# Performance work log

Measured on AMD Instinct MI355X. Metric: run time of the kernel, lower is better.

Reference implementation:

```python
import jax, jax.numpy as jnp
import numpy as np

STAGE_NUM = 3
BN_EPS = 1e-5


def _l2norm(x, axis):
    return x / (1e-6 + jnp.linalg.norm(x, axis=axis, keepdims=True))


def setup_inputs() -> dict:
    key = jax.random.key(0)
    b, c, k = 16, 256, 64
    sizes = [(80, 80), (40, 40), (20, 20), (10, 10)]
    ks = jax.random.split(key, 12)
    inp = {}
    for i, (h, w) in enumerate(sizes):
        inp[f"x{i}"] = jax.random.normal(ks[i], (b, c, h, w), dtype=jnp.float32)
    # 1x1 conv weights, kaiming-style init as in the module (n = out_channels)
    inp["w1"] = jax.random.normal(ks[8], (c, c), dtype=jnp.float32) * np.sqrt(2.0 / c)
    inp["b1"] = jnp.zeros((c,), dtype=jnp.float32)
    inp["w2"] = jax.random.normal(ks[9], (c, c), dtype=jnp.float32) * np.sqrt(2.0 / c)
    inp["bn_gamma"] = jnp.ones((c,), dtype=jnp.float32)
    inp["bn_beta"] = jnp.zeros((c,), dtype=jnp.float32)
    inp["bn_mean"] = jnp.zeros((c,), dtype=jnp.float32)
    inp["bn_var"] = jnp.ones((c,), dtype=jnp.float32)
    mu = jax.random.normal(ks[10], (1, c, k), dtype=jnp.float32) * np.sqrt(2.0 / k)
    inp["mu"] = _l2norm(mu, axis=1)
    return inp


def reference(x0, x1, x2, x3, w1, b1, w2, bn_gamma, bn_beta, bn_mean, bn_var, mu):
    xs = [x0, x1, x2, x3]
    b, c = x0.shape[0], x0.shape[1]
    idn = xs
    # conv1: 1x1 conv with bias == channel matmul
    xs = [jnp.einsum('oc,bchw->bohw', w1, x) + b1[None, :, None, None] for x in xs]
    sizes = [x.shape for x in xs]
    x_total = jnp.concatenate([x.reshape(b, c, -1) for x in xs], axis=-1)  # [b,c,N]
    k = mu.shape[-1]
    mu_b = jnp.broadcast_to(mu, (b, c, k))
    # EM iterations run under torch.no_grad() in the original -> stop_gradient
    xt = jax.lax.stop_gradient(x_total)
    z = None
    for _ in range(STAGE_NUM):
        z = jax.nn.softmax(jnp.einsum('bcn,bck->bnk', xt, mu_b), axis=2)  # [b,N,k]
        z_ = z / (1e-6 + z.sum(axis=1, keepdims=True))
        mu_b = _l2norm(jnp.einsum('bcn,bnk->bck', xt, z_), axis=1)
    # reconstruction: mu @ z^T, relu
    x_rec = jax.nn.relu(jnp.einsum('bck,bnk->bcn', mu_b, z))  # [b,c,N]
    outs = []
    cur = 0
    inv_std = (bn_gamma / jnp.sqrt(bn_var + BN_EPS))[None, :, None, None]
    shift = (bn_beta - bn_mean * bn_gamma / jnp.sqrt(bn_var + BN_EPS))[None, :, None, None]
    for i, s in enumerate(sizes):
        n = s[2] * s[3]
        term = x_rec[:, :, cur:cur + n].reshape(s)
        cur += n
        y = jnp.einsum('oc,bchw->bohw', w2, term)  # conv2 (no bias)
        y = y * inv_std + shift                    # eval-mode BatchNorm2d
        outs.append(jax.nn.relu(y + idn[i]))
    return (*outs, mu_b)
```

## Files before the change

kernel.cpp:

```cpp
#include <hip/hip_runtime.h>
#include <math.h>

#define NTOT 8500

__device__ __forceinline__ size_t in_index(int gn, int bc, int* which) {
  if (gn < 6400) { *which = 0; return (size_t)bc * 6400 + gn; }
  if (gn < 8000) { *which = 1; return (size_t)bc * 1600 + (gn - 6400); }
  if (gn < 8400) { *which = 2; return (size_t)bc * 400  + (gn - 8000); }
  *which = 3;     return (size_t)bc * 100  + (gn - 8400);
}

template <int WHICH>
__global__ __launch_bounds__(256)
void conv_kernel(const float* __restrict__ W, const float* __restrict__ bias,
                 const float* __restrict__ x0, const float* __restrict__ x1,
                 const float* __restrict__ x2, const float* __restrict__ x3,
                 const float* __restrict__ xrec,
                 const float* __restrict__ bn_g, const float* __restrict__ bn_b,
                 const float* __restrict__ bn_m, const float* __restrict__ bn_v,
                 float* __restrict__ out)
{
  __shared__ float As[32][68];
  __shared__ float Bs[32][132];
  const int t  = threadIdx.x;
  const int n0 = blockIdx.x * 128;
  const int m0 = blockIdx.y * 64;
  const int b  = blockIdx.z;
  const int tm = t & 15, tn = t >> 4;

  float acc[4][8];
#pragma unroll
  for (int i = 0; i < 4; ++i)
#pragma unroll
    for (int j = 0; j < 8; ++j) acc[i][j] = 0.f;

  for (int k0 = 0; k0 < 256; k0 += 32) {
#pragma unroll
    for (int it = 0; it < 2; ++it) {
      const int o_l = (t >> 3) + 32 * it;
      const int kk4 = (t & 7) * 4;
      float4 v = *(const float4*)(W + (size_t)(m0 + o_l) * 256 + k0 + kk4);
      As[kk4 + 0][o_l] = v.x; As[kk4 + 1][o_l] = v.y;
      As[kk4 + 2][o_l] = v.z; As[kk4 + 3][o_l] = v.w;
    }
#pragma unroll
    for (int it = 0; it < 4; ++it) {
      const int kk  = (t >> 5) + 8 * it;
      const int nn4 = (t & 31) * 4;
      const int gn  = n0 + nn4;
      float4 v = make_float4(0.f, 0.f, 0.f, 0.f);
      if (gn < NTOT) {
        if (WHICH == 0) {
          int w_; size_t idx = in_index(gn, b * 256 + k0 + kk, &w_);
          const float* src = (w_ == 0) ? x0 : (w_ == 1) ? x1 : (w_ == 2) ? x2 : x3;
          v = *(const float4*)(src + idx);
        } else {
          v = *(const float4*)(xrec + (size_t)(b * 256 + k0 + kk) * NTOT + gn);
        }
      }
      *(float4*)&Bs[kk][nn4] = v;
    }
    __syncthreads();
#pragma unroll
    for (int kk = 0; kk < 32; ++kk) {
      float4 a = *(const float4*)&As[kk][tm * 4];
      float4 p = *(const float4*)&Bs[kk][tn * 8];
      float4 q = *(const float4*)&Bs[kk][tn * 8 + 4];
      float av[4] = {a.x, a.y, a.z, a.w};
      float bv[8] = {p.x, p.y, p.z, p.w, q.x, q.y, q.z, q.w};
#pragma unroll
      for (int i = 0; i < 4; ++i)
#pragma unroll
        for (int j = 0; j < 8; ++j)
          acc[i][j] = fmaf(av[i], bv[j], acc[i][j]);
    }
    __syncthreads();
  }

#pragma unroll
  for (int i = 0; i < 4; ++i) {
    const int o = m0 + tm * 4 + i;
    float addb = 0.f, isf = 0.f, shf = 0.f;
    if (WHICH == 0) {
      addb = bias[o];
    } else {
      float g = bn_g[o];
      isf = g / sqrtf(bn_v[o] + 1e-5f);
      shf = bn_b[o] - bn_m[o] * isf;
    }
#pragma unroll
    for (int jj = 0; jj < 8; jj += 4) {
      const int gn = n0 + tn * 8 + jj;
      if (gn >= NTOT) continue;
      float4 r = make_float4(acc[i][jj + 0], acc[i][jj + 1],
                             acc[i][jj + 2], acc[i][jj + 3]);
      if (WHICH == 0) {
        r.x += addb; r.y += addb; r.z += addb; r.w += addb;
        *(float4*)(out + (size_t)(b * 256 + o) * NTOT + gn) = r;
      } else {
        int w_; size_t idx = in_index(gn, b * 256 + o, &w_);
        const float* src = (w_ == 0) ? x0 : (w_ == 1) ? x1 : (w_ == 2) ? x2 : x3;
        float4 rv = *(const float4*)(src + idx);
        size_t ob = (w_ == 0) ? 0ull : (w_ == 1) ? 26214400ull
                  : (w_ == 2) ? 32768000ull : 34406400ull;
        r.x = fmaxf(fmaf(r.x, isf, shf) + rv.x, 0.f);
        r.y = fmaxf(fmaf(r.y, isf, shf) + rv.y, 0.f);
        r.z = fmaxf(fmaf(r.z, isf, shf) + rv.z, 0.f);
        r.w = fmaxf(fmaf(r.w, isf, shf) + rv.w, 0.f);
        *(float4*)(out + ob + idx) = r;
      }
    }
  }
}

__global__ __launch_bounds__(256)
void z_kernel(const float* __restrict__ xt, const float* __restrict__ mu,
              int mu_per_batch, float* __restrict__ zbuf)
{
  __shared__ float xs[32][136];
  __shared__ float mus[32][68];
  const int t  = threadIdx.x;
  const int n0 = blockIdx.x * 128;
  const int b  = blockIdx.y;
  const float* mub = mu + (mu_per_batch ? (size_t)b * 256 * 64 : 0);
  const int tk = t & 15, tn = t >> 4;

  float acc[8][4];
#pragma unroll
  for (int r = 0; r < 8; ++r)
#pragma unroll
    for (int j = 0; j < 4; ++j) acc[r][j] = 0.f;

  for (int c0 = 0; c0 < 256; c0 += 32) {
#pragma unroll
    for (int it = 0; it < 4; ++it) {
      const int cc  = (t >> 5) + 8 * it;
      const int nn4 = (t & 31) * 4;
      const int gn  = n0 + nn4;
      float4 v = (gn < NTOT)
          ? *(const float4*)(xt + (size_t)(b * 256 + c0 + cc) * NTOT + gn)
          : make_float4(0.f, 0.f, 0.f, 0.f);
      *(float4*)&xs[cc][nn4] = v;
    }
#pragma unroll
    for (int it = 0; it < 2; ++it) {
      const int cc  = (t >> 4) + 16 * it;
      const int kk4 = (t & 15) * 4;
      float4 v = *(const float4*)(mub + (size_t)(c0 + cc) * 64 + kk4);
      *(float4*)&mus[cc][kk4] = v;
    }
    __syncthreads();
#pragma unroll
    for (int cc = 0; cc < 32; ++cc) {
      float4 m4 = *(const float4*)&mus[cc][tk * 4];
      float4 xa = *(const float4*)&xs[cc][tn * 8];
      float4 xb = *(const float4*)&xs[cc][tn * 8 + 4];
      float xv[8] = {xa.x, xa.y, xa.z, xa.w, xb.x, xb.y, xb.z, xb.w};
      float mv[4] = {m4.x, m4.y, m4.z, m4.w};
#pragma unroll
      for (int r = 0; r < 8; ++r)
#pragma unroll
        for (int j = 0; j < 4; ++j)
          acc[r][j] = fmaf(xv[r], mv[j], acc[r][j]);
    }
    __syncthreads();
  }

#pragma unroll
  for (int r = 0; r < 8; ++r) {
    float mx = fmaxf(fmaxf(acc[r][0], acc[r][1]), fmaxf(acc[r][2], acc[r][3]));
#pragma unroll
    for (int off = 8; off >= 1; off >>= 1) mx = fmaxf(mx, __shfl_xor(mx, off));
    float e0 = __expf(acc[r][0] - mx), e1 = __expf(acc[r][1] - mx);
    float e2 = __expf(acc[r][2] - mx), e3 = __expf(acc[r][3] - mx);
    float s = e0 + e1 + e2 + e3;
#pragma unroll
    for (int off = 8; off >= 1; off >>= 1) s += __shfl_xor(s, off);
    const float inv = 1.0f / s;
    const int gn = n0 + tn * 8 + r;
    if (gn < NTOT) {
      float4 w = make_float4(e0 * inv, e1 * inv, e2 * inv, e3 * inv);
      *(float4*)(zbuf + ((size_t)b * NTOT + gn) * 64 + tk * 4) = w;
    }
  }
}

__global__ __launch_bounds__(256)
void mu_part_kernel(const float* __restrict__ xt, const float* __restrict__ z,
                    float* __restrict__ part)
{
  __shared__ float As[32][132];
  __shared__ float Bs[32][68];
  const int t  = threadIdx.x;
  const int ch = blockIdx.x;
  const int c0 = blockIdx.y * 128;
  const int b  = blockIdx.z;
  const int nb = ch * 512;
  const int tk = t & 15, tc = t >> 4;

  float acc[8][4];
#pragma unroll
  for (int i = 0; i < 8; ++i)
#pragma unroll
    for (int j = 0; j < 4; ++j) acc[i][j] = 0.f;

  for (int kb = 0; kb < 512; kb += 32) {
#pragma unroll
    for (int it = 0; it < 4; ++it) {
      const int c_l = (t >> 3) + 32 * it;
      const int nn4 = (t & 7) * 4;
      const int gn  = nb + kb + nn4;
      float4 v = (gn < NTOT)
          ? *(const float4*)(xt + (size_t)(b * 256 + c0 + c_l) * NTOT + gn)
          : make_float4(0.f, 0.f, 0.f, 0.f);
      As[nn4 + 0][c_l] = v.x; As[nn4 + 1][c_l] = v.y;
      As[nn4 + 2][c_l] = v.z; As[nn4 + 3][c_l] = v.w;
    }
#pragma unroll
    for (int it = 0; it < 2; ++it) {
      const int nn  = (t >> 4) + 16 * it;
      const int kk4 = (t & 15) * 4;
      const int gn  = nb + kb + nn;
      float4 v = (gn < NTOT)
          ? *(const float4*)(z + ((size_t)b * NTOT + gn) * 64 + kk4)
          : make_float4(0.f, 0.f, 0.f, 0.f);
      *(float4*)&Bs[nn][kk4] = v;
    }
    __syncthreads();
#pragma unroll
    for (int nn = 0; nn < 32; ++nn) {
      float4 a0 = *(const float4*)&As[nn][tc * 8];
      float4 a1 = *(const float4*)&As[nn][tc * 8 + 4];
      float4 bz = *(const float4*)&Bs[nn][tk * 4];
      float av[8] = {a0.x, a0.y, a0.z, a0.w, a1.x, a1.y, a1.z, a1.w};
      float bv[4] = {bz.x, bz.y, bz.z, bz.w};
#pragma unroll
      for (int i = 0; i < 8; ++i)
#pragma unroll
        for (int j = 0; j < 4; ++j)
          acc[i][j] = fmaf(av[i], bv[j], acc[i][j]);
    }
    __syncthreads();
  }

#pragma unroll
  for (int j = 0; j < 4; ++j) {
    const int k = tk * 4 + j;
    float4 v0 = make_float4(acc[0][j], acc[1][j], acc[2][j], acc[3][j]);
    float4 v1 = make_float4(acc[4][j], acc[5][j], acc[6][j], acc[7][j]);
    size_t base = (((size_t)b * 17 + ch) * 64 + k) * 256 + c0 + tc * 8;
    *(float4*)(part + base)     = v0;
    *(float4*)(part + base + 4) = v1;
  }
}

__global__ __launch_bounds__(256)
void mu_reduce_kernel(const float* __restrict__ part, float* __restrict__ mu_ws,
                      float* __restrict__ mu_out)
{
  const int k = blockIdx.x;
  const int b = blockIdx.y;
  const int c = threadIdx.x;
  float s = 0.f;
  for (int ch = 0; ch < 17; ++ch)
    s += part[(((size_t)b * 17 + ch) * 64 + k) * 256 + c];
  __shared__ float red[256];
  red[c] = s * s;
  __syncthreads();
  for (int off = 128; off > 0; off >>= 1) {
    if (c < off) red[c] += red[c + off];
    __syncthreads();
  }
  const float f   = 1.0f / (1e-6f + sqrtf(red[0]));
  const float val = s * f;
  mu_ws[((size_t)b * 256 + c) * 64 + k] = val;
  if (mu_out) mu_out[((size_t)b * 256 + c) * 64 + k] = val;
}

__global__ __launch_bounds__(256)
void rec_kernel(const float* __restrict__ mu, const float* __restrict__ z,
                float* __restrict__ xrec)
{
  __shared__ float As[16][68];
  __shared__ float Bs[16][132];
  const int t  = threadIdx.x;
  const int n0 = blockIdx.x * 128;
  const int c0 = blockIdx.y * 64;
  const int b  = blockIdx.z;
  const int tm = t & 15, tn = t >> 4;

  float acc[4][8];
#pragma unroll
  for (int i = 0; i < 4; ++i)
#pragma unroll
    for (int j = 0; j < 8; ++j) acc[i][j] = 0.f;

  for (int k0 = 0; k0 < 64; k0 += 16) {
    {
      const int c_l = t >> 2;
      const int kk4 = (t & 3) * 4;
      float4 v = *(const float4*)(mu + ((size_t)(b * 256 + c0 + c_l)) * 64 + k0 + kk4);
      As[kk4 + 0][c_l] = v.x; As[kk4 + 1][c_l] = v.y;
      As[kk4 + 2][c_l] = v.z; As[kk4 + 3][c_l] = v.w;
    }
#pragma unroll
    for (int it = 0; it < 2; ++it) {
      const int nn  = (t >> 2) + 64 * it;
      const int kk4 = (t & 3) * 4;
      const int gn  = n0 + nn;
      float4 v = (gn < NTOT)
          ? *(const float4*)(z + ((size_t)b * NTOT + gn) * 64 + k0 + kk4)
          : make_float4(0.f, 0.f, 0.f, 0.f);
      Bs[kk4 + 0][nn] = v.x; Bs[kk4 + 1][nn] = v.y;
      Bs[kk4 + 2][nn] = v.z; Bs[kk4 + 3][nn] = v.w;
    }
    __syncthreads();
#pragma unroll
    for (int kk = 0; kk < 16; ++kk) {
      float4 a = *(const float4*)&As[kk][tm * 4];
      float4 p = *(const float4*)&Bs[kk][tn * 8];
      float4 q = *(const float4*)&Bs[kk][tn * 8 + 4];
      float av[4] = {a.x, a.y, a.z, a.w};
      float bv[8] = {p.x, p.y, p.z, p.w, q.x, q.y, q.z, q.w};
#pragma unroll
      for (int i = 0; i < 4; ++i)
#pragma unroll
        for (int j = 0; j < 8; ++j)
          acc[i][j] = fmaf(av[i], bv[j], acc[i][j]);
    }
    __syncthreads();
  }

#pragma unroll
  for (int i = 0; i < 4; ++i) {
    const int cc = c0 + tm * 4 + i;
#pragma unroll
    for (int jj = 0; jj < 8; jj += 4) {
      const int gn = n0 + tn * 8 + jj;
      if (gn >= NTOT) continue;
      float4 r = make_float4(fmaxf(acc[i][jj + 0], 0.f), fmaxf(acc[i][jj + 1], 0.f),
                             fmaxf(acc[i][jj + 2], 0.f), fmaxf(acc[i][jj + 3], 0.f));
      *(float4*)(xrec + (size_t)(b * 256 + cc) * NTOT + gn) = r;
    }
  }
}

extern "C" void kernel_launch(void* const* d_in, const int* in_sizes, int n_in,
                              void* d_out, int out_size, void* d_ws, size_t ws_size,
                              hipStream_t stream)
{
  const float* x0   = (const float*)d_in[0];
  const float* x1   = (const float*)d_in[1];
  const float* x2   = (const float*)d_in[2];
  const float* x3   = (const float*)d_in[3];
  const float* w1   = (const float*)d_in[4];
  const float* b1   = (const float*)d_in[5];
  const float* w2   = (const float*)d_in[6];
  const float* bn_g = (const float*)d_in[7];
  const float* bn_b = (const float*)d_in[8];
  const float* bn_m = (const float*)d_in[9];
  const float* bn_v = (const float*)d_in[10];
  const float* mu0  = (const float*)d_in[11];
  float* out = (float*)d_out;

  float* xt   = (float*)d_ws;
  float* z    = xt   + 34816000ull;
  float* part = z    + 8704000ull;
  float* muws = part + 4456448ull;

  dim3 gconv(67, 4, 16);
  conv_kernel<0><<<gconv, 256, 0, stream>>>(w1, b1, x0, x1, x2, x3,
                                            nullptr, nullptr, nullptr, nullptr,
                                            nullptr, xt);
  for (int s = 0; s < 3; ++s) {
    z_kernel<<<dim3(67, 16), 256, 0, stream>>>(xt, s == 0 ? mu0 : muws,
                                               s == 0 ? 0 : 1, z);
    mu_part_kernel<<<dim3(17, 2, 16), 256, 0, stream>>>(xt, z, part);
    mu_reduce_kernel<<<dim3(64, 16), 256, 0, stream>>>(
        part, muws, (s == 2) ? (out + 34816000ull) : nullptr);
  }
  rec_kernel<<<dim3(67, 4, 16), 256, 0, stream>>>(muws, z, xt);
  conv_kernel<1><<<gconv, 256, 0, stream>>>(w2, nullptr, x0, x1, x2, x3,
                                            xt, bn_g, bn_b, bn_m, bn_v, out);
}
```

Baseline: 1.232 ms.

## Eliminate conv1 by folding W1 and bias into EM projections

Removes the conv1 GEMM and its 139 MB xt intermediate. The EM iterations now work on the raw inputs. Scores use W1^T·mu plus a bias term, and mu updates apply W1 (plus b1 times the z column sums) to x·z. Small per-iteration kernels compute the transformed mu (t, s), and the column sums of z are accumulated inside mu_part. This trades a large GEMM and a full write/read of xt for extra small matvecs and gathers from the four input tensors, with slight changes in floating-point rounding.

Result: slower. 1.308 ms (+6.2%).

```diff
diff --git a/kernel.cpp b/kernel.cpp
--- a/kernel.cpp
+++ b/kernel.cpp
@@ -10,15 +10,14 @@
   *which = 3;     return (size_t)bc * 100  + (gn - 8400);
 }
 
-template <int WHICH>
-__global__ __launch_bounds__(256)
-void conv_kernel(const float* __restrict__ W, const float* __restrict__ bias,
-                 const float* __restrict__ x0, const float* __restrict__ x1,
-                 const float* __restrict__ x2, const float* __restrict__ x3,
-                 const float* __restrict__ xrec,
-                 const float* __restrict__ bn_g, const float* __restrict__ bn_b,
-                 const float* __restrict__ bn_m, const float* __restrict__ bn_v,
-                 float* __restrict__ out)
+__global__ __launch_bounds__(256)
+void conv2_kernel(const float* __restrict__ W,
+                  const float* __restrict__ x0, const float* __restrict__ x1,
+                  const float* __restrict__ x2, const float* __restrict__ x3,
+                  const float* __restrict__ xrec,
+                  const float* __restrict__ bn_g, const float* __restrict__ bn_b,
+                  const float* __restrict__ bn_m, const float* __restrict__ bn_v,
+                  float* __restrict__ out)
 {
   __shared__ float As[32][68];
   __shared__ float Bs[32][132];
@@ -49,15 +48,8 @@
       const int nn4 = (t & 31) * 4;
       const int gn  = n0 + nn4;
       float4 v = make_float4(0.f, 0.f, 0.f, 0.f);
-      if (gn < NTOT) {
-        if (WHICH == 0) {
-          int w_; size_t idx = in_index(gn, b * 256 + k0 + kk, &w_);
-          const float* src = (w_ == 0) ? x0 : (w_ == 1) ? x1 : (w_ == 2) ? x2 : x3;
-          v = *(const float4*)(src + idx);
-        } else {
-          v = *(const float4*)(xrec + (size_t)(b * 256 + k0 + kk) * NTOT + gn);
-        }
-      }
+      if (gn < NTOT)
+        v = *(const float4*)(xrec + (size_t)(b * 256 + k0 + kk) * NTOT + gn);
       *(float4*)&Bs[kk][nn4] = v;
     }
     __syncthreads();
@@ -80,50 +72,83 @@
 #pragma unroll
   for (int i = 0; i < 4; ++i) {
     const int o = m0 + tm * 4 + i;
-    float addb = 0.f, isf = 0.f, shf = 0.f;
-    if (WHICH == 0) {
-      addb = bias[o];
-    } else {
-      float g = bn_g[o];
-      isf = g / sqrtf(bn_v[o] + 1e-5f);
-      shf = bn_b[o] - bn_m[o] * isf;
-    }
+    float g   = bn_g[o];
+    float isf = g / sqrtf(bn_v[o] + 1e-5f);
+    float shf = bn_b[o] - bn_m[o] * isf;
 #pragma unroll
     for (int jj = 0; jj < 8; jj += 4) {
       const int gn = n0 + tn * 8 + jj;
       if (gn >= NTOT) continue;
       float4 r = make_float4(acc[i][jj + 0], acc[i][jj + 1],
                              acc[i][jj + 2], acc[i][jj + 3]);
-      if (WHICH == 0) {
-        r.x += addb; r.y += addb; r.z += addb; r.w += addb;
-        *(float4*)(out + (size_t)(b * 256 + o) * NTOT + gn) = r;
-      } else {
-        int w_; size_t idx = in_index(gn, b * 256 + o, &w_);
-        const float* src = (w_ == 0) ? x0 : (w_ == 1) ? x1 : (w_ == 2) ? x2 : x3;
-        float4 rv = *(const float4*)(src + idx);
-        size_t ob = (w_ == 0) ? 0ull : (w_ == 1) ? 26214400ull
-                  : (w_ == 2) ? 32768000ull : 34406400ull;
-        r.x = fmaxf(fmaf(r.x, isf, shf) + rv.x, 0.f);
-        r.y = fmaxf(fmaf(r.y, isf, shf) + rv.y, 0.f);
-        r.z = fmaxf(fmaf(r.z, isf, shf) + rv.z, 0.f);
-        r.w = fmaxf(fmaf(r.w, isf, shf) + rv.w, 0.f);
-        *(float4*)(out + ob + idx) = r;
-      }
-    }
-  }
-}
-
-__global__ __launch_bounds__(256)
-void z_kernel(const float* __restrict__ xt, const float* __restrict__ mu,
-              int mu_per_batch, float* __restrict__ zbuf)
+      int w_; size_t idx = in_index(gn, b * 256 + o, &w_);
+      const float* src = (w_ == 0) ? x0 : (w_ == 1) ? x1 : (w_ == 2) ? x2 : x3;
+      float4 rv = *(const float4*)(src + idx);
+      size_t ob = (w_ == 0) ? 0ull : (w_ == 1) ? 26214400ull
+                : (w_ == 2) ? 32768000ull : 34406400ull;
+      r.x = fmaxf(fmaf(r.x, isf, shf) + rv.x, 0.f);
+      r.y = fmaxf(fmaf(r.y, isf, shf) + rv.y, 0.f);
+      r.z = fmaxf(fmaf(r.z, isf, shf) + rv.z, 0.f);
+      r.w = fmaxf(fmaf(r.w, isf, shf) + rv.w, 0.f);
+      *(float4*)(out + ob + idx) = r;
+    }
+  }
+}
+
+__global__ __launch_bounds__(256)
+void transpose_kernel(const float* __restrict__ w1, float* __restrict__ w1t)
+{
+  __shared__ float tile[32][33];
+  const int bx = blockIdx.x, by = blockIdx.y;
+  const int tx = threadIdx.x & 31, ty = threadIdx.x >> 5;
+#pragma unroll
+  for (int j = 0; j < 32; j += 8)
+    tile[ty + j][tx] = w1[(size_t)(by * 32 + ty + j) * 256 + bx * 32 + tx];
+  __syncthreads();
+#pragma unroll
+  for (int j = 0; j < 32; j += 8)
+    w1t[(size_t)(bx * 32 + ty + j) * 256 + by * 32 + tx] = tile[tx][ty + j];
+}
+
+__global__ __launch_bounds__(256)
+void t0_kernel(const float* __restrict__ w1, const float* __restrict__ b1,
+               const float* __restrict__ mu0, float* __restrict__ t0,
+               float* __restrict__ s0)
+{
+  const int k = blockIdx.x, c = threadIdx.x;
+  __shared__ float M[256];
+  __shared__ float red[256];
+  M[c] = mu0[(size_t)c * 64 + k];
+  __syncthreads();
+  float acc = 0.f;
+#pragma unroll 8
+  for (int cp = 0; cp < 256; ++cp)
+    acc = fmaf(w1[(size_t)cp * 256 + c], M[cp], acc);
+  t0[(size_t)c * 64 + k] = acc;
+  red[c] = b1[c] * M[c];
+  __syncthreads();
+  for (int off = 128; off > 0; off >>= 1) {
+    if (c < off) red[c] += red[c + off];
+    __syncthreads();
+  }
+  if (c == 0) s0[k] = red[0];
+}
+
+__global__ __launch_bounds__(256)
+void z_kernel(const float* __restrict__ x0, const float* __restrict__ x1,
+              const float* __restrict__ x2, const float* __restrict__ x3,
+              const float* __restrict__ t, const float* __restrict__ s,
+              int per_batch, float* __restrict__ zbuf)
 {
   __shared__ float xs[32][136];
   __shared__ float mus[32][68];
-  const int t  = threadIdx.x;
+  const int tid = threadIdx.x;
   const int n0 = blockIdx.x * 128;
   const int b  = blockIdx.y;
-  const float* mub = mu + (mu_per_batch ? (size_t)b * 256 * 64 : 0);
-  const int tk = t & 15, tn = t >> 4;
+  const float* tb = t + (per_batch ? (size_t)b * 256 * 64 : 0);
+  const float* sb = s + (per_batch ? (size_t)b * 64 : 0);
+  const int tk = tid & 15, tn = tid >> 4;
+  const float4 sv = *(const float4*)(sb + tk * 4);
 
   float acc[8][4];
 #pragma unroll
@@ -134,19 +159,22 @@
   for (int c0 = 0; c0 < 256; c0 += 32) {
 #pragma unroll
     for (int it = 0; it < 4; ++it) {
-      const int cc  = (t >> 5) + 8 * it;
-      const int nn4 = (t & 31) * 4;
+      const int cc  = (tid >> 5) + 8 * it;
+      const int nn4 = (tid & 31) * 4;
       const int gn  = n0 + nn4;
-      float4 v = (gn < NTOT)
-          ? *(const float4*)(xt + (size_t)(b * 256 + c0 + cc) * NTOT + gn)
-          : make_float4(0.f, 0.f, 0.f, 0.f);
+      float4 v = make_float4(0.f, 0.f, 0.f, 0.f);
+      if (gn < NTOT) {
+        int w_; size_t idx = in_index(gn, b * 256 + c0 + cc, &w_);
+        const float* src = (w_ == 0) ? x0 : (w_ == 1) ? x1 : (w_ == 2) ? x2 : x3;
+        v = *(const float4*)(src + idx);
+      }
       *(float4*)&xs[cc][nn4] = v;
     }
 #pragma unroll
     for (int it = 0; it < 2; ++it) {
-      const int cc  = (t >> 4) + 16 * it;
-      const int kk4 = (t & 15) * 4;
-      float4 v = *(const float4*)(mub + (size_t)(c0 + cc) * 64 + kk4);
+      const int cc  = (tid >> 4) + 16 * it;
+      const int kk4 = (tid & 15) * 4;
+      float4 v = *(const float4*)(tb + (size_t)(c0 + cc) * 64 + kk4);
       *(float4*)&mus[cc][kk4] = v;
     }
     __syncthreads();
@@ -168,15 +196,16 @@
 
 #pragma unroll
   for (int r = 0; r < 8; ++r) {
+    acc[r][0] += sv.x; acc[r][1] += sv.y; acc[r][2] += sv.z; acc[r][3] += sv.w;
     float mx = fmaxf(fmaxf(acc[r][0], acc[r][1]), fmaxf(acc[r][2], acc[r][3]));
 #pragma unroll
     for (int off = 8; off >= 1; off >>= 1) mx = fmaxf(mx, __shfl_xor(mx, off));
     float e0 = __expf(acc[r][0] - mx), e1 = __expf(acc[r][1] - mx);
     float e2 = __expf(acc[r][2] - mx), e3 = __expf(acc[r][3] - mx);
-    float s = e0 + e1 + e2 + e3;
-#pragma unroll
-    for (int off = 8; off >= 1; off >>= 1) s += __shfl_xor(s, off);
-    const float inv = 1.0f / s;
+    float ssum = e0 + e1 + e2 + e3;
+#pragma unroll
+    for (int off = 8; off >= 1; off >>= 1) ssum += __shfl_xor(ssum, off);
+    const float inv = 1.0f / ssum;
     const int gn = n0 + tn * 8 + r;
     if (gn < NTOT) {
       float4 w = make_float4(e0 * inv, e1 * inv, e2 * inv, e3 * inv);
@@ -186,8 +215,10 @@
 }
 
 __global__ __launch_bounds__(256)
-void mu_part_kernel(const float* __restrict__ xt, const float* __restrict__ z,
-                    float* __restrict__ part)
+void mu_part_kernel(const float* __restrict__ x0, const float* __restrict__ x1,
+                    const float* __restrict__ x2, const float* __restrict__ x3,
+                    const float* __restrict__ z, float* __restrict__ part,
+                    float* __restrict__ csum)
 {
   __shared__ float As[32][132];
   __shared__ float Bs[32][68];
@@ -197,12 +228,14 @@
   const int b  = blockIdx.z;
   const int nb = ch * 512;
   const int tk = t & 15, tc = t >> 4;
+  const bool do_cs = (blockIdx.y == 0);
 
   float acc[8][4];
 #pragma unroll
   for (int i = 0; i < 8; ++i)
 #pragma unroll
     for (int j = 0; j < 4; ++j) acc[i][j] = 0.f;
+  float cs[4] = {0.f, 0.f, 0.f, 0.f};
 
   for (int kb = 0; kb < 512; kb += 32) {
 #pragma unroll
@@ -210,9 +243,12 @@
       const int c_l = (t >> 3) + 32 * it;
       const int nn4 = (t & 7) * 4;
       const int gn  = nb + kb + nn4;
-      float4 v = (gn < NTOT)
-          ? *(const float4*)(xt + (size_t)(b * 256 + c0 + c_l) * NTOT + gn)
-          : make_float4(0.f, 0.f, 0.f, 0.f);
+      float4 v = make_float4(0.f, 0.f, 0.f, 0.f);
+      if (gn < NTOT) {
+        int w_; size_t idx = in_index(gn, b * 256 + c0 + c_l, &w_);
+        const float* src = (w_ == 0) ? x0 : (w_ == 1) ? x1 : (w_ == 2) ? x2 : x3;
+        v = *(const float4*)(src + idx);
+      }
       As[nn4 + 0][c_l] = v.x; As[nn4 + 1][c_l] = v.y;
       As[nn4 + 2][c_l] = v.z; As[nn4 + 3][c_l] = v.w;
     }
@@ -227,6 +263,13 @@
       *(float4*)&Bs[nn][kk4] = v;
     }
     __syncthreads();
+    if (do_cs && tc == 0) {
+#pragma unroll
+      for (int nn = 0; nn < 32; ++nn) {
+#pragma unroll
+        for (int j = 0; j < 4; ++j) cs[j] += Bs[nn][tk * 4 + j];
+      }
+    }
 #pragma unroll
     for (int nn = 0; nn < 32; ++nn) {
       float4 a0 = *(const float4*)&As[nn][tc * 8];
@@ -252,29 +295,65 @@
     *(float4*)(part + base)     = v0;
     *(float4*)(part + base + 4) = v1;
   }
-}
-
-__global__ __launch_bounds__(256)
-void mu_reduce_kernel(const float* __restrict__ part, float* __restrict__ mu_ws,
-                      float* __restrict__ mu_out)
-{
-  const int k = blockIdx.x;
-  const int b = blockIdx.y;
-  const int c = threadIdx.x;
-  float s = 0.f;
+  if (do_cs && tc == 0) {
+#pragma unroll
+    for (int j = 0; j < 4; ++j)
+      csum[((size_t)b * 17 + ch) * 64 + tk * 4 + j] = cs[j];
+  }
+}
+
+__global__ __launch_bounds__(256)
+void mu_solve_kernel(const float* __restrict__ part, const float* __restrict__ csum,
+                     const float* __restrict__ w1t, const float* __restrict__ w1,
+                     const float* __restrict__ b1,
+                     float* __restrict__ muws, float* __restrict__ tbuf,
+                     float* __restrict__ sbuf, float* __restrict__ mu_out)
+{
+  const int k = blockIdx.x, b = blockIdx.y, c = threadIdx.x;
+  __shared__ float Y[256];
+  __shared__ float M[256];
+  __shared__ float red[256];
+
+  float y = 0.f;
   for (int ch = 0; ch < 17; ++ch)
-    s += part[(((size_t)b * 17 + ch) * 64 + k) * 256 + c];
-  __shared__ float red[256];
-  red[c] = s * s;
+    y += part[(((size_t)b * 17 + ch) * 64 + k) * 256 + c];
+  Y[c] = y;
+  float csv = 0.f;
+  for (int ch = 0; ch < 17; ++ch)
+    csv += csum[((size_t)b * 17 + ch) * 64 + k];
+  __syncthreads();
+
+  float acc = 0.f;
+#pragma unroll 8
+  for (int cp = 0; cp < 256; ++cp)
+    acc = fmaf(w1t[(size_t)cp * 256 + c], Y[cp], acc);
+  acc = fmaf(b1[c], csv, acc);
+
+  red[c] = acc * acc;
   __syncthreads();
   for (int off = 128; off > 0; off >>= 1) {
     if (c < off) red[c] += red[c + off];
     __syncthreads();
   }
-  const float f   = 1.0f / (1e-6f + sqrtf(red[0]));
-  const float val = s * f;
-  mu_ws[((size_t)b * 256 + c) * 64 + k] = val;
+  const float val = acc / (1e-6f + sqrtf(red[0]));
+  M[c] = val;
+  muws[((size_t)b * 256 + c) * 64 + k] = val;
   if (mu_out) mu_out[((size_t)b * 256 + c) * 64 + k] = val;
+  __syncthreads();
+
+  float acc2 = 0.f;
+#pragma unroll 8
+  for (int cp = 0; cp < 256; ++cp)
+    acc2 = fmaf(w1[(size_t)cp * 256 + c], M[cp], acc2);
+  tbuf[((size_t)b * 256 + c) * 64 + k] = acc2;
+
+  red[c] = b1[c] * val;
+  __syncthreads();
+  for (int off = 128; off > 0; off >>= 1) {
+    if (c < off) red[c] += red[c + off];
+    __syncthreads();
+  }
+  if (c == 0) sbuf[(size_t)b * 64 + k] = red[0];
 }
 
 __global__ __launch_bounds__(256)
@@ -363,23 +442,31 @@
   const float* mu0  = (const float*)d_in[11];
   float* out = (float*)d_out;
 
-  float* xt   = (float*)d_ws;
-  float* z    = xt   + 34816000ull;
+  float* xr   = (float*)d_ws;
+  float* z    = xr   + 34816000ull;
   float* part = z    + 8704000ull;
   float* muws = part + 4456448ull;
-
-  dim3 gconv(67, 4, 16);
-  conv_kernel<0><<<gconv, 256, 0, stream>>>(w1, b1, x0, x1, x2, x3,
-                                            nullptr, nullptr, nullptr, nullptr,
-                                            nullptr, xt);
+  float* tbuf = muws + 262144ull;
+  float* sbuf = tbuf + 262144ull;
+  float* t0b  = sbuf + 1024ull;
+  float* s0b  = t0b  + 16384ull;
+  float* csum = s0b  + 64ull;
+  float* w1t  = csum + 17408ull;
+
+  transpose_kernel<<<dim3(8, 8), 256, 0, stream>>>(w1, w1t);
+  t0_kernel<<<64, 256, 0, stream>>>(w1, b1, mu0, t0b, s0b);
+
   for (int s = 0; s < 3; ++s) {
-    z_kernel<<<dim3(67, 16), 256, 0, stream>>>(xt, s == 0 ? mu0 : muws,
-                                               s == 0 ? 0 : 1, z);
-    mu_part_kernel<<<dim3(17, 2, 16), 256, 0, stream>>>(xt, z, part);
-    mu_reduce_kernel<<<dim3(64, 16), 256, 0, stream>>>(
-        part, muws, (s == 2) ? (out + 34816000ull) : nullptr);
-  }
-  rec_kernel<<<dim3(67, 4, 16), 256, 0, stream>>>(muws, z, xt);
-  conv_kernel<1><<<gconv, 256, 0, stream>>>(w2, nullptr, x0, x1, x2, x3,
-                                            xt, bn_g, bn_b, bn_m, bn_v, out);
-}
+    z_kernel<<<dim3(67, 16), 256, 0, stream>>>(
+        x0, x1, x2, x3, s == 0 ? t0b : tbuf, s == 0 ? s0b : sbuf,
+        s == 0 ? 0 : 1, z);
+    mu_part_kernel<<<dim3(17, 2, 16), 256, 0, stream>>>(
+        x0, x1, x2, x3, z, part, csum);
+    mu_solve_kernel<<<dim3(64, 16), 256, 0, stream>>>(
+        part, csum, w1t, w1, b1, muws, tbuf, sbuf,
+        (s == 2) ? (out + 34816000ull) : nullptr);
+  }
+  rec_kernel<<<dim3(67, 4, 16), 256, 0, stream>>>(muws, z, xr);
+  conv2_kernel<<<dim3(67, 4, 16), 256, 0, stream>>>(
+      w2, x0, x1, x2, x3, xr, bn_g, bn_b, bn_m, bn_v, out);
+}
```
